# Optimization experiments

Measured on AMD Instinct MI355X. Metric: run time of the kernel, lower is better.

The kernel has to match this reference:

```python
import jax, jax.numpy as jnp
import numpy as np

B, S, D, H, MEM, P = 32, 512, 768, 8, 768, 3
DK = D // H
LN_EPS = 1e-6


def _layer_norm(x, a, b):
    # torch LayerNorm in source uses unbiased std (ddof=1) and adds eps to std
    mean = x.mean(-1, keepdims=True)
    var = ((x - mean) ** 2).sum(-1, keepdims=True) / (x.shape[-1] - 1)
    return a * (x - mean) / (jnp.sqrt(var) + LN_EPS) + b


def _gcn_branch(x, mask, Wq, bq, Wk, bk, Ws, bs):
    # x: [B,S,D], mask: [B,S] 0/1 ints
    q = (x @ Wq.T + bq).reshape(B, S, H, DK).transpose(0, 2, 1, 3)  # [B,H,S,DK]
    k = (x @ Wk.T + bk).reshape(B, S, H, DK).transpose(0, 2, 1, 3)
    scores = jnp.einsum('bhqd,bhkd->bhqk', q, k) / jnp.sqrt(jnp.float32(DK))
    scores = jnp.where(mask[:, None, None, :] == 0, jnp.float32(-1e9), scores)
    adj = jax.nn.softmax(scores, axis=-1).mean(1)  # average heads -> [B,S,S]
    # adj - diag(diag(adj)) + I  ==  set diagonal to 1
    idx = jnp.arange(S)
    adj = adj.at[:, idx, idx].set(1.0)
    adj = adj * mask[:, :, None].astype(adj.dtype)  # src_mask.transpose(1,2) * adj
    denom = adj.sum(-1, keepdims=True) + 1.0
    out = x
    for W, b in zip(Ws, bs):
        out = jax.nn.relu((adj @ out @ W.T + b) / denom)
    return out, adj


def _proj(a, b):
    # Proj(a, b): (a.b / |b|) * normalize(b)
    b_mo = jnp.sqrt((b * b).sum(-1))
    axb = (a * b).sum(-1)
    bn = b / jnp.maximum(jnp.sqrt((b * b).sum(-1, keepdims=True)), 1e-12)
    return (axb / b_mo)[:, None] * bn


def setup_inputs() -> dict:
    key = jax.random.key(0)
    ks = jax.random.split(key, 32)

    def w(k, shape):
        return jax.random.normal(k, shape, jnp.float32) * 0.02

    inp = {
        'sequence_output': jax.random.normal(ks[0], (B, S, D), jnp.float32),
        'pooled_output': jax.random.normal(ks[1], (B, D), jnp.float32),
        'src_mask': jnp.ones((B, S), jnp.int32),
        'aspect_mask': jnp.ones((B, S), jnp.float32),
        'ln_a': jnp.ones((D,), jnp.float32),
        'ln_b': jnp.zeros((D,), jnp.float32),
        'fp_Wq': w(ks[2], (D, D)), 'fp_bq': jnp.zeros((D,), jnp.float32),
        'fp_Wk': w(ks[3], (D, D)), 'fp_bk': jnp.zeros((D,), jnp.float32),
        'fp_W0': w(ks[4], (MEM, D)), 'fp_b0': jnp.zeros((MEM,), jnp.float32),
        'fp_W1': w(ks[5], (MEM, MEM)), 'fp_b1': jnp.zeros((MEM,), jnp.float32),
        'fc_Wq': w(ks[6], (D, D)), 'fc_bq': jnp.zeros((D,), jnp.float32),
        'fc_Wk': w(ks[7], (D, D)), 'fc_bk': jnp.zeros((D,), jnp.float32),
        'fc_W0': w(ks[8], (MEM, D)), 'fc_b0': jnp.zeros((MEM,), jnp.float32),
        'fc_W1': w(ks[9], (MEM, MEM)), 'fc_b1': jnp.zeros((MEM,), jnp.float32),
        'fp_dense_W': w(ks[10], (P, MEM)), 'fp_dense_b': jnp.zeros((P,), jnp.float32),
        'fc_dense_W': w(ks[11], (P, MEM)), 'fc_dense_b': jnp.zeros((P,), jnp.float32),
    }
    return inp


def reference(sequence_output, pooled_output, src_mask, aspect_mask,
              ln_a, ln_b,
              fp_Wq, fp_bq, fp_Wk, fp_bk, fp_W0, fp_b0, fp_W1, fp_b1,
              fc_Wq, fc_bq, fc_Wk, fc_bk, fc_W0, fc_b0, fc_W1, fc_b1,
              fp_dense_W, fp_dense_b, fc_dense_W, fc_dense_b):
    label_embedding = pooled_output
    att_inputs = _layer_norm(sequence_output, ln_a, ln_b)  # dropout disabled (eval)
    asp_wn = aspect_mask.sum(1)[:, None]  # [B,1]

    fp_out, _ = _gcn_branch(att_inputs, src_mask, fp_Wq, fp_bq, fp_Wk, fp_bk,
                            [fp_W0, fp_W1], [fp_b0, fp_b1])
    fc_out, _ = _gcn_branch(att_inputs, src_mask, fc_Wq, fc_bq, fc_Wk, fc_bk,
                            [fc_W0, fc_W1], [fc_b0, fc_b1])

    outputs_fp = fp_out.sum(1)  # [B,MEM]
    outputs_fc = (fc_out * aspect_mask[:, :, None]).sum(1) / asp_wn  # [B,MEM]

    fp_x = _proj(outputs_fp, outputs_fc)
    fp_y = _proj(outputs_fp, outputs_fp - fp_x)
    fc_y = outputs_fc  # gradient-reverse layer is identity in forward

    logits_p = fp_y @ fp_dense_W.T + fp_dense_b
    logits_c = fc_y @ fc_dense_W.T + fc_dense_b
    return (logits_p, logits_c, fp_y, label_embedding)
```

## Files before the change

kernel.cpp:

```cpp
#include <hip/hip_runtime.h>
#include <math.h>
#include <stdint.h>

#define Bn 32
#define Sn 512
#define Dn 768
#define Hn 8
#define DKn 96
#define Pn 3

typedef __bf16 bf16_t;
typedef bf16_t bf16x8 __attribute__((ext_vector_type(8)));
typedef float f32x4 __attribute__((ext_vector_type(4)));

__device__ __forceinline__ bf16_t f2bf(float f) { return (bf16_t)f; }

__device__ __forceinline__ void gload16(const void* g, void* l) {
    __builtin_amdgcn_global_load_lds((const __attribute__((address_space(1))) void*)g,
                                     (__attribute__((address_space(3))) void*)l, 16, 0, 0);
}

__device__ __forceinline__ float brsum(float v, float* red) {
    int t = threadIdx.x;
    red[t] = v; __syncthreads();
    #pragma unroll
    for (int o = 128; o > 0; o >>= 1) {
        if (t < o) red[t] += red[t + o];
        __syncthreads();
    }
    float r = red[0]; __syncthreads();
    return r;
}

__global__ __launch_bounds__(256) void ln_kernel(const float* __restrict__ in,
                                                 const float* __restrict__ ga,
                                                 const float* __restrict__ gb,
                                                 bf16_t* __restrict__ out) {
    __shared__ float red[256];
    long row = blockIdx.x;
    const float* x = in + row * Dn;
    bf16_t* y = out + row * Dn;
    int t = threadIdx.x;
    float v0 = x[t], v1 = x[t + 256], v2 = x[t + 512];
    float mean = brsum(v0 + v1 + v2, red) / (float)Dn;
    float d0 = v0 - mean, d1 = v1 - mean, d2 = v2 - mean;
    float ss = brsum(d0 * d0 + d1 * d1 + d2 * d2, red);
    float inv = 1.0f / (sqrtf(ss / (float)(Dn - 1)) + 1e-6f);
    y[t]       = f2bf(ga[t]       * d0 * inv + gb[t]);
    y[t + 256] = f2bf(ga[t + 256] * d1 * inv + gb[t + 256]);
    y[t + 512] = f2bf(ga[t + 512] * d2 * inv + gb[t + 512]);
}

__global__ __launch_bounds__(256) void cvt4(const float* __restrict__ s0,
                                            const float* __restrict__ s1,
                                            const float* __restrict__ s2,
                                            const float* __restrict__ s3,
                                            bf16_t* __restrict__ dst) {
    const float* s = (blockIdx.y == 0) ? s0 : (blockIdx.y == 1) ? s1 : (blockIdx.y == 2) ? s2 : s3;
    long i = (long)blockIdx.x * 1024 + threadIdx.x * 4;
    float4 v = *reinterpret_cast<const float4*>(s + i);
    bf16_t* d = dst + (long)blockIdx.y * Dn * Dn + i;
    d[0] = f2bf(v.x); d[1] = f2bf(v.y); d[2] = f2bf(v.z); d[3] = f2bf(v.w);
}

__global__ void zero_kernel(float* p, int n) {
    int i = blockIdx.x * 256 + threadIdx.x;
    if (i < n) p[i] = 0.0f;
}

template <int EPI>
__global__ __launch_bounds__(256) void gemm_bt(
    const bf16_t* __restrict__ Ag, const bf16_t* __restrict__ Bg,
    bf16_t* __restrict__ Cg, float* __restrict__ outv,
    int lda, int ldb, int ldc, int K,
    long sA1, long sB1, long sC1,
    float alpha,
    const float* __restrict__ bias,
    const float* __restrict__ bias2,
    const float* __restrict__ denom,
    const float* __restrict__ aspw) {
    __shared__ __align__(16) bf16_t As[128 * 32];
    __shared__ __align__(16) bf16_t Bs[128 * 32];

    int zb = blockIdx.z;
    const bf16_t* A = Ag + zb * sA1;
    const bf16_t* B = Bg + zb * sB1;

    int n0 = blockIdx.x * 128;
    int m0 = blockIdx.y * 128;
    int tid = threadIdx.x;
    int lane = tid & 63, wv = tid >> 6;
    int wm = wv >> 1, wn = wv & 1;

    int sub = lane >> 2;
    int kcol = (lane & 3) * 8;
    const bf16_t* pA0 = A + (size_t)(m0 + wv * 16 + sub) * lda + kcol;
    const bf16_t* pA1 = pA0 + (size_t)64 * lda;
    const bf16_t* pB0 = B + (size_t)(n0 + wv * 16 + sub) * ldb + kcol;
    const bf16_t* pB1 = pB0 + (size_t)64 * ldb;
    bf16_t* lA0 = As + wv * 512 + lane * 8;
    bf16_t* lA1 = As + (4 + wv) * 512 + lane * 8;
    bf16_t* lB0 = Bs + wv * 512 + lane * 8;
    bf16_t* lB1 = Bs + (4 + wv) * 512 + lane * 8;

    f32x4 acc[4][4];
    #pragma unroll
    for (int i = 0; i < 4; i++)
        #pragma unroll
        for (int j = 0; j < 4; j++) acc[i][j] = (f32x4){0.f, 0.f, 0.f, 0.f};

    const bf16_t* ar = As + (wm * 64 + (lane & 15)) * 32 + (lane >> 4) * 8;
    const bf16_t* br = Bs + (wn * 64 + (lane & 15)) * 32 + (lane >> 4) * 8;

    for (int k0 = 0; k0 < K; k0 += 32) {
        gload16(pA0 + k0, lA0);
        gload16(pA1 + k0, lA1);
        gload16(pB0 + k0, lB0);
        gload16(pB1 + k0, lB1);
        __syncthreads();
        bf16x8 a[4], b[4];
        #pragma unroll
        for (int i = 0; i < 4; i++) a[i] = *(const bf16x8*)(ar + i * 16 * 32);
        #pragma unroll
        for (int j = 0; j < 4; j++) b[j] = *(const bf16x8*)(br + j * 16 * 32);
        #pragma unroll
        for (int i = 0; i < 4; i++)
            #pragma unroll
            for (int j = 0; j < 4; j++)
                acc[i][j] = __builtin_amdgcn_mfma_f32_16x16x32_bf16(a[i], b[j], acc[i][j], 0, 0, 0);
        __syncthreads();
    }

    int nb = n0 + wn * 64 + (lane & 15);
    int mbase = m0 + wm * 64 + (lane >> 4) * 4;

    if (EPI == 0) {
        bf16_t* Cz = Cg + zb * sC1;
        #pragma unroll
        for (int i = 0; i < 4; i++) {
            #pragma unroll
            for (int r = 0; r < 4; r++) {
                long m = mbase + i * 16 + r;
                bf16_t* crow = Cz + m * (long)ldc;
                #pragma unroll
                for (int j = 0; j < 4; j++) {
                    int col = nb + j * 16;
                    float v = acc[i][j][r] * alpha;
                    if (bias2) v += (col < Dn) ? bias[col] : bias2[col - Dn];
                    else if (bias) v += bias[col];
                    crow[col] = f2bf(v);
                }
            }
        }
    } else if (EPI == 1) {
        bf16_t* Cz = Cg + zb * sC1;
        const float* dz = denom + (long)zb * Sn;
        #pragma unroll
        for (int i = 0; i < 4; i++) {
            #pragma unroll
            for (int r = 0; r < 4; r++) {
                int m = mbase + i * 16 + r;
                float dinv = 1.0f / dz[m];
                bf16_t* crow = Cz + (long)m * ldc;
                #pragma unroll
                for (int j = 0; j < 4; j++) {
                    float v = fmaxf((acc[i][j][r] + bias[nb + j * 16]) * dinv, 0.0f);
                    crow[nb + j * 16] = f2bf(v);
                }
            }
        }
    } else {
        const float* dz = denom + (long)zb * Sn;
        float csum[4] = {0.f, 0.f, 0.f, 0.f};
        #pragma unroll
        for (int i = 0; i < 4; i++) {
            #pragma unroll
            for (int r = 0; r < 4; r++) {
                int m = mbase + i * 16 + r;
                float dinv = 1.0f / dz[m];
                float w = aspw ? aspw[(long)zb * Sn + m] : 1.0f;
                #pragma unroll
                for (int j = 0; j < 4; j++) {
                    float v = fmaxf((acc[i][j][r] + bias[nb + j * 16]) * dinv, 0.0f);
                    csum[j] += v * w;
                }
            }
        }
        #pragma unroll
        for (int j = 0; j < 4; j++) {
            float s = csum[j];
            s += __shfl_xor(s, 16);
            s += __shfl_xor(s, 32);
            if (lane < 16) atomicAdd(&outv[(long)zb * Dn + nb + j * 16], s);
        }
    }
}

__global__ __launch_bounds__(256) void fused_adj(
    const bf16_t* __restrict__ QK, bf16_t* __restrict__ adjb,
    float* __restrict__ denomv, const int* __restrict__ mask) {
    __shared__ __align__(16) bf16_t Ks[2][128 * 104];
    __shared__ float red[4][16];

    int L = blockIdx.x;
    int b = (L & 7) * 4 + ((L >> 3) >> 4);
    int q0 = ((L >> 3) & 15) * 32;

    int tid = threadIdx.x;
    int lane = tid & 63, w = tid >> 6;
    int mt = w >> 1, nh = w & 1;
    int g = lane >> 4, c = lane & 15;

    const int LDQ = 2 * Dn;
    const bf16_t* Qrow  = QK + ((long)b * Sn + q0 + mt * 16 + c) * LDQ;
    const bf16_t* Kbase = QK + (long)b * Sn * LDQ + Dn;

    const int* mrow = mask + (long)b * Sn;
    unsigned mbits = 0;
    #pragma unroll
    for (int t = 0; t < 4; ++t)
        #pragma unroll
        for (int nj = 0; nj < 4; ++nj)
            if (mrow[t * 128 + nh * 64 + nj * 16 + c] != 0) mbits |= 1u << (t * 4 + nj);

    int srow[6], scc[6];
    #pragma unroll
    for (int p = 0; p < 6; ++p) { int gr = tid + p * 256; srow[p] = gr / 12; scc[p] = gr % 12; }

    f32x4 adjacc[4][4];
    #pragma unroll
    for (int t = 0; t < 4; ++t)
        #pragma unroll
        for (int nj = 0; nj < 4; ++nj) adjacc[t][nj] = (f32x4){0.f, 0.f, 0.f, 0.f};

    f32x4 S[4][4];
    bf16x8 kr0[6], kr1[6], aq[3], aqn[3];
    const float sal = 0.102062072615966f;

    #pragma unroll
    for (int p = 0; p < 6; ++p)
        kr0[p] = *(const bf16x8*)(Kbase + (long)srow[p] * LDQ + scc[p] * 8);
    #pragma unroll
    for (int ks = 0; ks < 3; ++ks)
        aq[ks] = *(const bf16x8*)(Qrow + ks * 32 + g * 8);
    #pragma unroll
    for (int p = 0; p < 6; ++p)
        *(bf16x8*)(&Ks[0][srow[p] * 104 + scc[p] * 8]) = kr0[p];
    #pragma unroll
    for (int p = 0; p < 6; ++p)
        kr1[p] = *(const bf16x8*)(Kbase + (long)(128 + srow[p]) * LDQ + scc[p] * 8);
    __syncthreads();

    for (int h = 0; h < Hn; ++h) {
        #pragma unroll
        for (int t = 0; t < 4; ++t)
            #pragma unroll
            for (int nj = 0; nj < 4; ++nj) S[t][nj] = (f32x4){0.f, 0.f, 0.f, 0.f};

        float rs[4];
        #pragma unroll
        for (int t = 0; t < 4; ++t) {
            int it = h * 4 + t;
            if (it + 2 < 32) {
                int nt = it + 2;
                const bf16_t* kp = Kbase + (long)((nt & 3) * 128) * LDQ + (nt >> 2) * 96;
                if ((t & 1) == 0) {
                    #pragma unroll
                    for (int p = 0; p < 6; ++p)
                        kr0[p] = *(const bf16x8*)(kp + (long)srow[p] * LDQ + scc[p] * 8);
                } else {
                    #pragma unroll
                    for (int p = 0; p < 6; ++p)
                        kr1[p] = *(const bf16x8*)(kp + (long)srow[p] * LDQ + scc[p] * 8);
                }
            }
            if (t == 2 && h < 7) {
                #pragma unroll
                for (int ks = 0; ks < 3; ++ks)
                    aqn[ks] = *(const bf16x8*)(Qrow + (h + 1) * 96 + ks * 32 + g * 8);
            }
            #pragma unroll
            for (int nj = 0; nj < 4; ++nj) {
                #pragma unroll
                for (int ks = 0; ks < 3; ++ks) {
                    bf16x8 bk = *(const bf16x8*)(&Ks[t & 1][(nh * 64 + nj * 16 + c) * 104 + ks * 32 + g * 8]);
                    S[t][nj] = __builtin_amdgcn_mfma_f32_16x16x32_bf16(aq[ks], bk, S[t][nj], 0, 0, 0);
                }
            }
            if (t == 3) {
                rs[0] = rs[1] = rs[2] = rs[3] = 0.f;
                #pragma unroll
                for (int tt = 0; tt < 4; ++tt)
                    #pragma unroll
                    for (int nj = 0; nj < 4; ++nj) {
                        float mkf = ((mbits >> (tt * 4 + nj)) & 1u) ? 1.0f : 0.0f;
                        #pragma unroll
                        for (int ri = 0; ri < 4; ++ri) {
                            float e = mkf * __expf(S[tt][nj][ri] * sal);
                            S[tt][nj][ri] = e;
                            rs[ri] += e;
                        }
                    }
                #pragma unroll
                for (int ri = 0; ri < 4; ++ri) {
                    rs[ri] += __shfl_xor(rs[ri], 1);
                    rs[ri] += __shfl_xor(rs[ri], 2);
                    rs[ri] += __shfl_xor(rs[ri], 4);
                    rs[ri] += __shfl_xor(rs[ri], 8);
                }
                if (c == 0) {
                    #pragma unroll
                    for (int ri = 0; ri < 4; ++ri) red[w][g * 4 + ri] = rs[ri];
                }
            }
            if (it + 1 < 32) {
                if ((t & 1) == 0) {
                    #pragma unroll
                    for (int p = 0; p < 6; ++p)
                        *(bf16x8*)(&Ks[1][srow[p] * 104 + scc[p] * 8]) = kr1[p];
                } else {
                    #pragma unroll
                    for (int p = 0; p < 6; ++p)
                        *(bf16x8*)(&Ks[0][srow[p] * 104 + scc[p] * 8]) = kr0[p];
                }
            }
            __syncthreads();
            if (t == 3) {
                float inv[4];
                #pragma unroll
                for (int ri = 0; ri < 4; ++ri)
                    inv[ri] = 0.125f / (red[w][g * 4 + ri] + red[w ^ 1][g * 4 + ri]);
                #pragma unroll
                for (int tt = 0; tt < 4; ++tt)
                    #pragma unroll
                    for (int nj = 0; nj < 4; ++nj)
                        #pragma unroll
                        for (int ri = 0; ri < 4; ++ri)
                            adjacc[tt][nj][ri] += S[tt][nj][ri] * inv[ri];
                if (h < 7) {
                    #pragma unroll
                    for (int ks = 0; ks < 3; ++ks) aq[ks] = aqn[ks];
                }
            }
        }
    }

    float rm[4];
    #pragma unroll
    for (int ri = 0; ri < 4; ++ri)
        rm[ri] = (mrow[q0 + mt * 16 + g * 4 + ri] != 0) ? 1.0f : 0.0f;
    float rs2[4] = {0.f, 0.f, 0.f, 0.f};
    #pragma unroll
    for (int t = 0; t < 4; ++t)
        #pragma unroll
        for (int nj = 0; nj < 4; ++nj) {
            int n = t * 128 + nh * 64 + nj * 16 + c;
            #pragma unroll
            for (int ri = 0; ri < 4; ++ri) {
                float v = adjacc[t][nj][ri];
                int q = q0 + mt * 16 + g * 4 + ri;
                if (n == q) v = 1.0f;
                v *= rm[ri];
                adjacc[t][nj][ri] = v;
                rs2[ri] += v;
            }
        }
    #pragma unroll
    for (int ri = 0; ri < 4; ++ri) {
        rs2[ri] += __shfl_xor(rs2[ri], 1);
        rs2[ri] += __shfl_xor(rs2[ri], 2);
        rs2[ri] += __shfl_xor(rs2[ri], 4);
        rs2[ri] += __shfl_xor(rs2[ri], 8);
    }
    __syncthreads();
    if (c == 0) {
        #pragma unroll
        for (int ri = 0; ri < 4; ++ri) red[w][g * 4 + ri] = rs2[ri];
    }
    __syncthreads();
    if (nh == 0 && c == 0) {
        #pragma unroll
        for (int ri = 0; ri < 4; ++ri)
            denomv[(long)b * Sn + q0 + mt * 16 + g * 4 + ri] =
                red[w][g * 4 + ri] + red[w ^ 1][g * 4 + ri] + 1.0f;
    }
    bf16_t* stg = &Ks[0][0];
    #pragma unroll
    for (int t = 0; t < 4; ++t)
        #pragma unroll
        for (int nj = 0; nj < 4; ++nj) {
            int n = t * 128 + nh * 64 + nj * 16 + c;
            #pragma unroll
            for (int ri = 0; ri < 4; ++ri)
                stg[(mt * 16 + g * 4 + ri) * 520 + n] = f2bf(adjacc[t][nj][ri]);
        }
    __syncthreads();
    bf16_t* arow = adjb + ((long)b * Sn + q0) * Sn;
    #pragma unroll
    for (int p = 0; p < 8; ++p) {
        int gr = tid + p * 256;
        int row = gr >> 6, cc = gr & 63;
        *(bf16x8*)(arow + (long)row * Sn + cc * 8) = *(const bf16x8*)(stg + row * 520 + cc * 8);
    }
}

__global__ __launch_bounds__(256) void final_kernel(const float* __restrict__ ofp,
                                                    const float* __restrict__ ofc_raw,
                                                    const float* __restrict__ aspect,
                                                    const float* __restrict__ pooled,
                                                    const float* __restrict__ fpdW,
                                                    const float* __restrict__ fpdb,
                                                    const float* __restrict__ fcdW,
                                                    const float* __restrict__ fcdb,
                                                    float* __restrict__ out) {
    __shared__ float red[256];
    __shared__ float fp[Dn], fc[Dn], fy[Dn];
    int b = blockIdx.x, t = threadIdx.x;
    float awv = aspect[(long)b * Sn + t] + aspect[(long)b * Sn + t + 256];
    float asp_wn = brsum(awv, red);
    for (int i = t; i < Dn; i += 256) {
        fp[i] = ofp[(long)b * Dn + i];
        fc[i] = ofc_raw[(long)b * Dn + i] / asp_wn;
    }
    __syncthreads();
    float p0 = 0.0f, p1 = 0.0f;
    for (int i = t; i < Dn; i += 256) { p0 += fc[i] * fc[i]; p1 += fp[i] * fc[i]; }
    float dfc2 = brsum(p0, red);
    float dfpfc = brsum(p1, red);
    float bmo = sqrtf(dfc2);
    float coef = dfpfc / bmo;
    float bden = fmaxf(bmo, 1e-12f);
    float q0 = 0.0f, q1 = 0.0f;
    for (int i = t; i < Dn; i += 256) {
        float tv = fp[i] - coef * fc[i] / bden;
        fy[i] = tv;
        q0 += tv * tv;
        q1 += fp[i] * tv;
    }
    float dt2 = brsum(q0, red);
    float dfpt = brsum(q1, red);
    float tmo = sqrtf(dt2);
    float coef2 = dfpt / tmo;
    float tden = fmaxf(tmo, 1e-12f);
    for (int i = t; i < Dn; i += 256) fy[i] = coef2 * fy[i] / tden;
    __syncthreads();
    for (int i = t; i < Dn; i += 256) out[2 * Bn * Pn + (long)b * Dn + i] = fy[i];
    for (int i = t; i < Dn; i += 256)
        out[2 * Bn * Pn + Bn * Dn + (long)b * Dn + i] = pooled[(long)b * Dn + i];
    for (int j = 0; j < Pn; j++) {
        float lp = 0.0f, lc = 0.0f;
        for (int i = t; i < Dn; i += 256) {
            lp += fy[i] * fpdW[(long)j * Dn + i];
            lc += fc[i] * fcdW[(long)j * Dn + i];
        }
        float rp = brsum(lp, red);
        float rc = brsum(lc, red);
        if (t == 0) {
            out[(long)b * Pn + j] = rp + fpdb[j];
            out[Bn * Pn + (long)b * Pn + j] = rc + fcdb[j];
        }
    }
}

extern "C" void kernel_launch(void* const* d_in, const int* in_sizes, int n_in,
                              void* d_out, int out_size, void* d_ws, size_t ws_size,
                              hipStream_t stream) {
    const float* seq     = (const float*)d_in[0];
    const float* pooled  = (const float*)d_in[1];
    const int*   src_msk = (const int*)d_in[2];
    const float* aspect  = (const float*)d_in[3];
    const float* ln_a    = (const float*)d_in[4];
    const float* ln_b    = (const float*)d_in[5];
    float* out = (float*)d_out;

    const long NTD = (long)Bn * Sn * Dn;
    const long NSS = (long)Bn * Sn * Sn;
    const long DD  = (long)Dn * Dn;

    char* w = (char*)d_ws;
    bf16_t* xbf   = (bf16_t*)w;
    bf16_t* QK    = xbf + NTD;
    bf16_t* adjb  = QK + 2 * NTD;
    float*  denom = (float*)(adjb + NSS);
    float*  ofp   = denom + (long)Bn * Sn;
    float*  ofc   = ofp + (long)Bn * Dn;
    bf16_t* Wb    = (bf16_t*)(ofc + (long)Bn * Dn);
    bf16_t* XT    = Wb + 4 * DD;

    ln_kernel<<<dim3(Bn * Sn), dim3(256), 0, stream>>>(seq, ln_a, ln_b, xbf);
    zero_kernel<<<dim3((2 * Bn * Dn + 255) / 256), dim3(256), 0, stream>>>(ofp, 2 * Bn * Dn);

    for (int br = 0; br < 2; ++br) {
        const float* Wq = (const float*)d_in[6 + br * 8 + 0];
        const float* bq = (const float*)d_in[6 + br * 8 + 1];
        const float* Wk = (const float*)d_in[6 + br * 8 + 2];
        const float* bk = (const float*)d_in[6 + br * 8 + 3];
        const float* W0 = (const float*)d_in[6 + br * 8 + 4];
        const float* b0 = (const float*)d_in[6 + br * 8 + 5];
        const float* W1 = (const float*)d_in[6 + br * 8 + 6];
        const float* b1 = (const float*)d_in[6 + br * 8 + 7];
        float* outv = (br == 0) ? ofp : ofc;

        cvt4<<<dim3(576, 4), dim3(256), 0, stream>>>(Wq, Wk, W0, W1, Wb);

        gemm_bt<0><<<dim3(12, 128, 1), dim3(256), 0, stream>>>(
            xbf, Wb, QK, nullptr, Dn, Dn, 2 * Dn, Dn,
            0, 0, 0, 1.0f, bq, bk, nullptr, nullptr);

        fused_adj<<<dim3(Bn * Sn / 32), dim3(256), 0, stream>>>(
            QK, adjb, denom, src_msk);

        gemm_bt<0><<<dim3(4, 6, Bn), dim3(256), 0, stream>>>(
            Wb + 2 * DD, xbf, XT, nullptr, Dn, Dn, Sn, Dn,
            0, (long)Sn * Dn, (long)Dn * Sn,
            1.0f, nullptr, nullptr, nullptr, nullptr);

        gemm_bt<1><<<dim3(6, 4, Bn), dim3(256), 0, stream>>>(
            adjb, XT, QK, nullptr, Sn, Sn, Dn, Sn,
            (long)Sn * Sn, (long)Dn * Sn, (long)Sn * Dn,
            1.0f, b0, nullptr, denom, nullptr);

        gemm_bt<0><<<dim3(4, 6, Bn), dim3(256), 0, stream>>>(
            Wb + 3 * DD, QK, XT, nullptr, Dn, Dn, Sn, Dn,
            0, (long)Sn * Dn, (long)Dn * Sn,
            1.0f, nullptr, nullptr, nullptr, nullptr);

        gemm_bt<2><<<dim3(6, 4, Bn), dim3(256), 0, stream>>>(
            adjb, XT, nullptr, outv, Sn, Sn, 0, Sn,
            (long)Sn * Sn, (long)Dn * Sn, 0,
            1.0f, b1, nullptr, denom, (br == 1) ? aspect : nullptr);
    }

    final_kernel<<<dim3(Bn), dim3(256), 0, stream>>>(
        ofp, ofc, aspect, pooled,
        (const float*)d_in[22], (const float*)d_in[23],
        (const float*)d_in[24], (const float*)d_in[25], out);
}
```

Before: 616.7 us.

## Batch both GCN branches into single launches with XCD-aware block swizzle

Merges the fp and fc branches so that each stage (QK projection, adjacency, two GCN layers) runs as one launch covering both branches. It does this by concatenating weights and biases and adding a branch index to the grid's z dimension. A chiplet (XCD) swizzle remaps block indices so that neighbouring tiles land on the same XCD for L2 reuse. The aim is to cut launch count and raise per-launch occupancy. In exchange, workspace use doubles for adjacency and intermediates, and stride arithmetic gets more complex.

```diff
diff --git a/kernel.cpp b/kernel.cpp
--- a/kernel.cpp
+++ b/kernel.cpp
@@ -51,16 +51,37 @@
     y[t + 512] = f2bf(ga[t + 512] * d2 * inv + gb[t + 512]);
 }
 
-__global__ __launch_bounds__(256) void cvt4(const float* __restrict__ s0,
+__global__ __launch_bounds__(256) void cvt8(const float* __restrict__ s0,
                                             const float* __restrict__ s1,
                                             const float* __restrict__ s2,
                                             const float* __restrict__ s3,
+                                            const float* __restrict__ s4,
+                                            const float* __restrict__ s5,
+                                            const float* __restrict__ s6,
+                                            const float* __restrict__ s7,
                                             bf16_t* __restrict__ dst) {
-    const float* s = (blockIdx.y == 0) ? s0 : (blockIdx.y == 1) ? s1 : (blockIdx.y == 2) ? s2 : s3;
+    int y = blockIdx.y;
+    const float* s = (y == 0) ? s0 : (y == 1) ? s1 : (y == 2) ? s2 : (y == 3) ? s3
+                   : (y == 4) ? s4 : (y == 5) ? s5 : (y == 6) ? s6 : s7;
     long i = (long)blockIdx.x * 1024 + threadIdx.x * 4;
     float4 v = *reinterpret_cast<const float4*>(s + i);
-    bf16_t* d = dst + (long)blockIdx.y * Dn * Dn + i;
+    bf16_t* d = dst + (long)y * Dn * Dn + i;
     d[0] = f2bf(v.x); d[1] = f2bf(v.y); d[2] = f2bf(v.z); d[3] = f2bf(v.w);
+}
+
+__global__ __launch_bounds__(256) void biascat_k(const float* __restrict__ s0,
+                                                 const float* __restrict__ s1,
+                                                 const float* __restrict__ s2,
+                                                 const float* __restrict__ s3,
+                                                 const float* __restrict__ s4,
+                                                 const float* __restrict__ s5,
+                                                 const float* __restrict__ s6,
+                                                 const float* __restrict__ s7,
+                                                 float* __restrict__ dst) {
+    int y = blockIdx.x;
+    const float* s = (y == 0) ? s0 : (y == 1) ? s1 : (y == 2) ? s2 : (y == 3) ? s3
+                   : (y == 4) ? s4 : (y == 5) ? s5 : (y == 6) ? s6 : s7;
+    for (int i = threadIdx.x; i < Dn; i += 256) dst[(long)y * Dn + i] = s[i];
 }
 
 __global__ void zero_kernel(float* p, int n) {
@@ -73,21 +94,33 @@
     const bf16_t* __restrict__ Ag, const bf16_t* __restrict__ Bg,
     bf16_t* __restrict__ Cg, float* __restrict__ outv,
     int lda, int ldb, int ldc, int K,
-    long sA1, long sB1, long sC1,
-    float alpha,
-    const float* __restrict__ bias,
-    const float* __restrict__ bias2,
+    long sAhi, long sAlo, long sBhi, long sBlo, long sChi, long sClo,
+    int lgZ, float alpha,
+    const float* __restrict__ bias, long bias_zs,
     const float* __restrict__ denom,
     const float* __restrict__ aspw) {
     __shared__ __align__(16) bf16_t As[128 * 32];
     __shared__ __align__(16) bf16_t Bs[128 * 32];
 
-    int zb = blockIdx.z;
-    const bf16_t* A = Ag + zb * sA1;
-    const bf16_t* B = Bg + zb * sB1;
-
-    int n0 = blockIdx.x * 128;
-    int m0 = blockIdx.y * 128;
+    unsigned gx = gridDim.x, gy = gridDim.y;
+    unsigned nwg = gx * gy * gridDim.z;
+    unsigned flat = (blockIdx.z * gy + blockIdx.y) * gx + blockIdx.x;
+    unsigned q8 = nwg >> 3, r8 = nwg & 7;
+    unsigned xcd = flat & 7, idx = flat >> 3;
+    unsigned swz = (xcd < r8 ? xcd * (q8 + 1) : r8 * (q8 + 1) + (xcd - r8) * q8) + idx;
+    unsigned bx = swz % gx;
+    unsigned rest = swz / gx;
+    unsigned by = rest % gy;
+    unsigned zz = rest / gy;
+    int zb = zz >> lgZ;
+    int zg = zz & ((1 << lgZ) - 1);
+    long zful = ((long)zb << lgZ) + zg;
+
+    const bf16_t* A = Ag + zb * sAhi + zg * sAlo;
+    const bf16_t* B = Bg + zb * sBhi + zg * sBlo;
+
+    int n0 = bx * 128;
+    int m0 = by * 128;
     int tid = threadIdx.x;
     int lane = tid & 63, wv = tid >> 6;
     int wm = wv >> 1, wn = wv & 1;
@@ -133,9 +166,10 @@
 
     int nb = n0 + wn * 64 + (lane & 15);
     int mbase = m0 + wm * 64 + (lane >> 4) * 4;
+    const float* bz = bias ? bias + zb * bias_zs : nullptr;
 
     if (EPI == 0) {
-        bf16_t* Cz = Cg + zb * sC1;
+        bf16_t* Cz = Cg + zb * sChi + zg * sClo;
         #pragma unroll
         for (int i = 0; i < 4; i++) {
             #pragma unroll
@@ -146,15 +180,14 @@
                 for (int j = 0; j < 4; j++) {
                     int col = nb + j * 16;
                     float v = acc[i][j][r] * alpha;
-                    if (bias2) v += (col < Dn) ? bias[col] : bias2[col - Dn];
-                    else if (bias) v += bias[col];
+                    if (bz) v += bz[col];
                     crow[col] = f2bf(v);
                 }
             }
         }
     } else if (EPI == 1) {
-        bf16_t* Cz = Cg + zb * sC1;
-        const float* dz = denom + (long)zb * Sn;
+        bf16_t* Cz = Cg + zb * sChi + zg * sClo;
+        const float* dz = denom + zful * Sn;
         #pragma unroll
         for (int i = 0; i < 4; i++) {
             #pragma unroll
@@ -164,13 +197,13 @@
                 bf16_t* crow = Cz + (long)m * ldc;
                 #pragma unroll
                 for (int j = 0; j < 4; j++) {
-                    float v = fmaxf((acc[i][j][r] + bias[nb + j * 16]) * dinv, 0.0f);
+                    float v = fmaxf((acc[i][j][r] + bz[nb + j * 16]) * dinv, 0.0f);
                     crow[nb + j * 16] = f2bf(v);
                 }
             }
         }
     } else {
-        const float* dz = denom + (long)zb * Sn;
+        const float* dz = denom + zful * Sn;
         float csum[4] = {0.f, 0.f, 0.f, 0.f};
         #pragma unroll
         for (int i = 0; i < 4; i++) {
@@ -178,11 +211,11 @@
             for (int r = 0; r < 4; r++) {
                 int m = mbase + i * 16 + r;
                 float dinv = 1.0f / dz[m];
-                float w = aspw ? aspw[(long)zb * Sn + m] : 1.0f;
+                float wgt = (aspw && zb) ? aspw[(long)zg * Sn + m] : 1.0f;
                 #pragma unroll
                 for (int j = 0; j < 4; j++) {
-                    float v = fmaxf((acc[i][j][r] + bias[nb + j * 16]) * dinv, 0.0f);
-                    csum[j] += v * w;
+                    float v = fmaxf((acc[i][j][r] + bz[nb + j * 16]) * dinv, 0.0f);
+                    csum[j] += v * wgt;
                 }
             }
         }
@@ -191,7 +224,7 @@
             float s = csum[j];
             s += __shfl_xor(s, 16);
             s += __shfl_xor(s, 32);
-            if (lane < 16) atomicAdd(&outv[(long)zb * Dn + nb + j * 16], s);
+            if (lane < 16) atomicAdd(&outv[zful * Dn + nb + j * 16], s);
         }
     }
 }
@@ -203,17 +236,20 @@
     __shared__ float red[4][16];
 
     int L = blockIdx.x;
-    int b = (L & 7) * 4 + ((L >> 3) >> 4);
-    int q0 = ((L >> 3) & 15) * 32;
+    int swzi = (L & 7) * 128 + (L >> 3);
+    int brc = swzi >> 9;
+    int rem = swzi & 511;
+    int b = rem >> 4;
+    int q0 = (rem & 15) * 32;
 
     int tid = threadIdx.x;
     int lane = tid & 63, w = tid >> 6;
     int mt = w >> 1, nh = w & 1;
     int g = lane >> 4, c = lane & 15;
 
-    const int LDQ = 2 * Dn;
-    const bf16_t* Qrow  = QK + ((long)b * Sn + q0 + mt * 16 + c) * LDQ;
-    const bf16_t* Kbase = QK + (long)b * Sn * LDQ + Dn;
+    const int LDQ = 3072;
+    const bf16_t* Qrow  = QK + ((long)b * Sn + q0 + mt * 16 + c) * LDQ + brc * 1536;
+    const bf16_t* Kbase = QK + (long)b * Sn * LDQ + brc * 1536 + Dn;
 
     const int* mrow = mask + (long)b * Sn;
     unsigned mbits = 0;
@@ -378,10 +414,11 @@
         for (int ri = 0; ri < 4; ++ri) red[w][g * 4 + ri] = rs2[ri];
     }
     __syncthreads();
+    long zful = (long)brc * Bn + b;
     if (nh == 0 && c == 0) {
         #pragma unroll
         for (int ri = 0; ri < 4; ++ri)
-            denomv[(long)b * Sn + q0 + mt * 16 + g * 4 + ri] =
+            denomv[zful * Sn + q0 + mt * 16 + g * 4 + ri] =
                 red[w][g * 4 + ri] + red[w ^ 1][g * 4 + ri] + 1.0f;
     }
     bf16_t* stg = &Ks[0][0];
@@ -395,7 +432,7 @@
                 stg[(mt * 16 + g * 4 + ri) * 520 + n] = f2bf(adjacc[t][nj][ri]);
         }
     __syncthreads();
-    bf16_t* arow = adjb + ((long)b * Sn + q0) * Sn;
+    bf16_t* arow = adjb + (zful * Sn + q0) * Sn;
     #pragma unroll
     for (int p = 0; p < 8; ++p) {
         int gr = tid + p * 256;
@@ -476,63 +513,61 @@
     const long NTD = (long)Bn * Sn * Dn;
     const long NSS = (long)Bn * Sn * Sn;
     const long DD  = (long)Dn * Dn;
+    const long SD  = (long)Sn * Dn;
 
     char* w = (char*)d_ws;
     bf16_t* xbf   = (bf16_t*)w;
     bf16_t* QK    = xbf + NTD;
-    bf16_t* adjb  = QK + 2 * NTD;
-    float*  denom = (float*)(adjb + NSS);
-    float*  ofp   = denom + (long)Bn * Sn;
-    float*  ofc   = ofp + (long)Bn * Dn;
-    bf16_t* Wb    = (bf16_t*)(ofc + (long)Bn * Dn);
-    bf16_t* XT    = Wb + 4 * DD;
+    bf16_t* H1    = QK;
+    bf16_t* XT    = QK + 2 * NTD;
+    bf16_t* adjb  = QK + 4 * NTD;
+    float*  denom = (float*)(adjb + 2 * NSS);
+    float*  ofp   = denom + 2L * Bn * Sn;
+    float*  bcat  = ofp + 2L * Bn * Dn;
+    bf16_t* Wb    = (bf16_t*)(bcat + 8 * Dn);
 
     ln_kernel<<<dim3(Bn * Sn), dim3(256), 0, stream>>>(seq, ln_a, ln_b, xbf);
     zero_kernel<<<dim3((2 * Bn * Dn + 255) / 256), dim3(256), 0, stream>>>(ofp, 2 * Bn * Dn);
 
-    for (int br = 0; br < 2; ++br) {
-        const float* Wq = (const float*)d_in[6 + br * 8 + 0];
-        const float* bq = (const float*)d_in[6 + br * 8 + 1];
-        const float* Wk = (const float*)d_in[6 + br * 8 + 2];
-        const float* bk = (const float*)d_in[6 + br * 8 + 3];
-        const float* W0 = (const float*)d_in[6 + br * 8 + 4];
-        const float* b0 = (const float*)d_in[6 + br * 8 + 5];
-        const float* W1 = (const float*)d_in[6 + br * 8 + 6];
-        const float* b1 = (const float*)d_in[6 + br * 8 + 7];
-        float* outv = (br == 0) ? ofp : ofc;
-
-        cvt4<<<dim3(576, 4), dim3(256), 0, stream>>>(Wq, Wk, W0, W1, Wb);
-
-        gemm_bt<0><<<dim3(12, 128, 1), dim3(256), 0, stream>>>(
-            xbf, Wb, QK, nullptr, Dn, Dn, 2 * Dn, Dn,
-            0, 0, 0, 1.0f, bq, bk, nullptr, nullptr);
-
-        fused_adj<<<dim3(Bn * Sn / 32), dim3(256), 0, stream>>>(
-            QK, adjb, denom, src_msk);
-
-        gemm_bt<0><<<dim3(4, 6, Bn), dim3(256), 0, stream>>>(
-            Wb + 2 * DD, xbf, XT, nullptr, Dn, Dn, Sn, Dn,
-            0, (long)Sn * Dn, (long)Dn * Sn,
-            1.0f, nullptr, nullptr, nullptr, nullptr);
-
-        gemm_bt<1><<<dim3(6, 4, Bn), dim3(256), 0, stream>>>(
-            adjb, XT, QK, nullptr, Sn, Sn, Dn, Sn,
-            (long)Sn * Sn, (long)Dn * Sn, (long)Sn * Dn,
-            1.0f, b0, nullptr, denom, nullptr);
-
-        gemm_bt<0><<<dim3(4, 6, Bn), dim3(256), 0, stream>>>(
-            Wb + 3 * DD, QK, XT, nullptr, Dn, Dn, Sn, Dn,
-            0, (long)Sn * Dn, (long)Dn * Sn,
-            1.0f, nullptr, nullptr, nullptr, nullptr);
-
-        gemm_bt<2><<<dim3(6, 4, Bn), dim3(256), 0, stream>>>(
-            adjb, XT, nullptr, outv, Sn, Sn, 0, Sn,
-            (long)Sn * Sn, (long)Dn * Sn, 0,
-            1.0f, b1, nullptr, denom, (br == 1) ? aspect : nullptr);
-    }
+    cvt8<<<dim3(576, 8), dim3(256), 0, stream>>>(
+        (const float*)d_in[6], (const float*)d_in[8],
+        (const float*)d_in[14], (const float*)d_in[16],
+        (const float*)d_in[10], (const float*)d_in[18],
+        (const float*)d_in[12], (const float*)d_in[20], Wb);
+    biascat_k<<<dim3(8), dim3(256), 0, stream>>>(
+        (const float*)d_in[7], (const float*)d_in[9],
+        (const float*)d_in[15], (const float*)d_in[17],
+        (const float*)d_in[11], (const float*)d_in[19],
+        (const float*)d_in[13], (const float*)d_in[21], bcat);
+
+    gemm_bt<0><<<dim3(24, 128, 1), dim3(256), 0, stream>>>(
+        xbf, Wb, QK, nullptr, Dn, Dn, 3072, Dn,
+        0, 0, 0, 0, 0, 0, 0, 1.0f, bcat, 0, nullptr, nullptr);
+
+    fused_adj<<<dim3(2 * Bn * Sn / 32), dim3(256), 0, stream>>>(QK, adjb, denom, src_msk);
+
+    gemm_bt<0><<<dim3(4, 6, 64), dim3(256), 0, stream>>>(
+        Wb + 4 * DD, xbf, XT, nullptr, Dn, Dn, Sn, Dn,
+        DD, 0, 0, SD, 32 * SD, SD,
+        5, 1.0f, nullptr, 0, nullptr, nullptr);
+
+    gemm_bt<1><<<dim3(6, 4, 64), dim3(256), 0, stream>>>(
+        adjb, XT, H1, nullptr, Sn, Sn, Dn, Sn,
+        32L * Sn * Sn, (long)Sn * Sn, 32 * SD, SD, 32 * SD, SD,
+        5, 1.0f, bcat + 4 * Dn, Dn, denom, nullptr);
+
+    gemm_bt<0><<<dim3(4, 6, 64), dim3(256), 0, stream>>>(
+        Wb + 6 * DD, H1, XT, nullptr, Dn, Dn, Sn, Dn,
+        DD, 0, 32 * SD, SD, 32 * SD, SD,
+        5, 1.0f, nullptr, 0, nullptr, nullptr);
+
+    gemm_bt<2><<<dim3(6, 4, 64), dim3(256), 0, stream>>>(
+        adjb, XT, nullptr, ofp, Sn, Sn, 0, Sn,
+        32L * Sn * Sn, (long)Sn * Sn, 32 * SD, SD, 0, 0,
+        5, 1.0f, bcat + 6 * Dn, Dn, denom, aspect);
 
     final_kernel<<<dim3(Bn), dim3(256), 0, stream>>>(
-        ofp, ofc, aspect, pooled,
+        ofp, ofp + (long)Bn * Dn, aspect, pooled,
         (const float*)d_in[22], (const float*)d_in[23],
         (const float*)d_in[24], (const float*)d_in[25], out);
 }
```

Result: faster. 516.6 us (-16.2%).
